# Kernel tuning notes

Measured on AMD Instinct MI355X. Metric: run time of the kernel, lower is better.

## Reference

```python
import jax, jax.numpy as jnp
import numpy as np

QLEN, B, D = 1024, 4, 512
H, DH = 8, 64
MEM, DMLP = 1024, 2048
KLEN = MEM + QLEN
EPS = 1e-5


def layer_norm(x, g, b):
    mu = jnp.mean(x, axis=-1, keepdims=True)
    var = jnp.var(x, axis=-1, keepdims=True)
    return (x - mu) * jax.lax.rsqrt(var + EPS) * g + b


def rel_shift(x):
    # x: [qlen, klen, b, h] -- Transformer-XL relative shift trick
    q, k, b, h = x.shape
    zp = jnp.zeros((q, 1, b, h), dtype=x.dtype)
    x = jnp.concatenate([zp, x], axis=1)          # [q, k+1, b, h]
    x = x.reshape(k + 1, q, b, h)[1:]             # drop first row
    return x.reshape(q, k, b, h)


def setup_inputs() -> dict:
    key = jax.random.key(0)
    ks = jax.random.split(key, 12)
    s = 0.02
    inp = {
        "inputs": jax.random.normal(ks[0], (QLEN, B, D), jnp.float32),
        "r": jax.random.normal(ks[1], (KLEN, D), jnp.float32),
        "u": jax.random.normal(ks[2], (H, DH), jnp.float32) * s,
        "v": jax.random.normal(ks[3], (H, DH), jnp.float32) * s,
        "mem": jax.random.normal(ks[4], (MEM, B, D), jnp.float32),
        # causal mask: query i (global pos MEM+i) cannot attend key j > MEM+i
        "attn_mask": jnp.arange(KLEN)[None, :] > (jnp.arange(QLEN)[:, None] + MEM),
        "Wqkv": jax.random.normal(ks[5], (3 * D, D), jnp.float32) * s,
        "Wr": jax.random.normal(ks[6], (D, D), jnp.float32) * s,
        "Wo": jax.random.normal(ks[7], (D, D), jnp.float32) * s,
        "ln1_g": jnp.ones((D,), jnp.float32),
        "ln1_b": jnp.zeros((D,), jnp.float32),
        "mlp_w1": jax.random.normal(ks[8], (DMLP, D), jnp.float32) * s,
        "mlp_b1": jnp.zeros((DMLP,), jnp.float32),
        "mlp_w2": jax.random.normal(ks[9], (D, DMLP), jnp.float32) * s,
        "mlp_b2": jnp.zeros((D,), jnp.float32),
        "ln2_g": jnp.ones((D,), jnp.float32),
        "ln2_b": jnp.zeros((D,), jnp.float32),
    }
    return inp


def reference(inputs, r, u, v, mem, attn_mask, Wqkv, Wr, Wo,
              ln1_g, ln1_b, mlp_w1, mlp_b1, mlp_w2, mlp_b2, ln2_g, ln2_b):
    qlen, b, d = inputs.shape
    cat = jnp.concatenate([mem, inputs], axis=0)          # [klen, b, d]
    klen = cat.shape[0]
    qkv = cat @ Wqkv.T                                    # [klen, b, 3d]
    q, k, w_v = jnp.split(qkv, 3, axis=-1)
    q = q[-qlen:].reshape(qlen, b, H, DH)
    k = k.reshape(klen, b, H, DH)
    w_v = w_v.reshape(klen, b, H, DH)
    rk = (r @ Wr.T).reshape(klen, H, DH)                  # [klen, h, dh]

    AC = jnp.einsum('ibhd,jbhd->ijbh', q + u, k)          # content term
    BD = jnp.einsum('ibhd,jhd->ijbh', q + v, rk)          # position term
    BD = rel_shift(BD)
    scale = 1.0 / np.sqrt(DH)
    score = (AC + BD) * scale                             # [q, k, b, h]
    score = jnp.where(attn_mask[:, :, None, None], jnp.float32(-1e30), score)
    prob = jax.nn.softmax(score, axis=1)
    attn = jnp.einsum('ijbh,jbhd->ibhd', prob, w_v).reshape(qlen, b, d)
    attn_out = attn @ Wo.T

    y = layer_norm(inputs + attn_out, ln1_g, ln1_b)
    h = jax.nn.relu(y @ mlp_w1.T + mlp_b1)
    z = h @ mlp_w2.T + mlp_b2
    out = layer_norm(y + z, ln2_g, ln2_b)
    return out, prob
```

## Files before the change

kernel.cpp:

```cpp
#include <hip/hip_runtime.h>
#include <math.h>

#define QL 1024
#define BSZ 4
#define DM 512
#define NH 8
#define DHH 64
#define MEML 1024
#define KL 2048
#define DMLP 2048

typedef __attribute__((ext_vector_type(8))) short bf16x8;
typedef __attribute__((ext_vector_type(4))) float f32x4;

#define MFMA16(A, B, C) __builtin_amdgcn_mfma_f32_16x16x32_bf16((A), (B), (C), 0, 0, 0)
#define SWZB(r, cb) (((r) << 7) + ((cb) ^ (((r) & 7) << 4)))
#define RINGB(r, c) (((r) << 9) + ((((c) << 2)) ^ (((r) & 7) << 4)))
#define CVT2(dst, lo, hi) \
  asm("v_cvt_pk_bf16_f32 %0, %1, %2" : "=v"(dst) : "v"(lo), "v"(hi))
#define GLOAD_LDS(gp, lp) __builtin_amdgcn_global_load_lds( \
    (const __attribute__((address_space(1))) void*)(gp), \
    (__attribute__((address_space(3))) void*)(lp), 16, 0, 0)

__device__ __forceinline__ unsigned short bf16_1(float x) {
  unsigned int t; CVT2(t, x, x); return (unsigned short)t;
}
__device__ __forceinline__ void split1(float x, unsigned short& h, unsigned short& l) {
  unsigned int th; CVT2(th, x, x);
  h = (unsigned short)th;
  const float r = x - __uint_as_float(((unsigned int)h) << 16);
  unsigned int tl; CVT2(tl, r, r);
  l = (unsigned short)tl;
}

__device__ __forceinline__ void split_bf16(const float4 a, uint2& h, uint2& l) {
  CVT2(h.x, a.x, a.y); CVT2(h.y, a.z, a.w);
  float r;
  float4 rr;
  rr.x = a.x - __uint_as_float(h.x << 16);
  rr.y = a.y - __uint_as_float(h.x & 0xffff0000u);
  rr.z = a.z - __uint_as_float(h.y << 16);
  rr.w = a.w - __uint_as_float(h.y & 0xffff0000u);
  CVT2(l.x, rr.x, rr.y); CVT2(l.y, rr.z, rr.w);
  (void)r;
}

__device__ __forceinline__ void store_tiled(char* hiB, char* loB, int KT,
                                            int row, int c0, uint2 h, uint2 l) {
  const size_t off = (((size_t)(row >> 7) * KT + (c0 >> 6)) << 14)
                   + SWZB(row & 127, (c0 & 63) * 2);
  *(uint2*)(hiB + off) = h;
  *(uint2*)(loB + off) = l;
}

__global__ __launch_bounds__(256)
void precvt_all(const float* __restrict__ mem, const float* __restrict__ inputs,
                const float* __restrict__ r, const float* __restrict__ Wqkv,
                const float* __restrict__ Wr, const float* __restrict__ Wo,
                const float* __restrict__ w1, const float* __restrict__ w2,
                unsigned short* CAThi, unsigned short* CATlo,
                unsigned short* Rhi, unsigned short* Rlo,
                unsigned short* Qhi, unsigned short* Qlo,
                unsigned short* WrHi, unsigned short* WrLo,
                unsigned short* WoHi, unsigned short* WoLo,
                unsigned short* w1Hi, unsigned short* w1Lo,
                unsigned short* w2Hi, unsigned short* w2Lo) {
  const int id = blockIdx.x * 256 + threadIdx.x;
  float4 a; uint2 h, l;
  if (id < 1048576) {
    const int row = id >> 7, c0 = (id & 127) * 4;
    const float* s = (row < 4096) ? mem + (size_t)row * 512
                                  : inputs + (size_t)(row - 4096) * 512;
    a = *(const float4*)(s + c0);
    split_bf16(a, h, l);
    store_tiled((char*)CAThi, (char*)CATlo, 8, row, c0, h, l);
  } else if (id < 1310720) {
    const int e = id - 1048576, row = e >> 7, c0 = (e & 127) * 4;
    a = *(const float4*)(r + (size_t)row * 512 + c0);
    split_bf16(a, h, l);
    store_tiled((char*)Rhi, (char*)Rlo, 8, row, c0, h, l);
  } else if (id < 1507328) {
    const int e = id - 1310720, row = e >> 7, c0 = (e & 127) * 4;
    a = *(const float4*)(Wqkv + (size_t)row * 512 + c0);
    split_bf16(a, h, l);
    store_tiled((char*)Qhi, (char*)Qlo, 8, row, c0, h, l);
  } else if (id < 1572864) {
    const int e = id - 1507328, row = e >> 7, c0 = (e & 127) * 4;
    a = *(const float4*)(Wr + (size_t)row * 512 + c0);
    split_bf16(a, h, l);
    store_tiled((char*)WrHi, (char*)WrLo, 8, row, c0, h, l);
  } else if (id < 1638400) {
    const int e = id - 1572864, row = e >> 7, c0 = (e & 127) * 4;
    a = *(const float4*)(Wo + (size_t)row * 512 + c0);
    split_bf16(a, h, l);
    store_tiled((char*)WoHi, (char*)WoLo, 8, row, c0, h, l);
  } else if (id < 1900544) {
    const int e = id - 1638400, row = e >> 7, c0 = (e & 127) * 4;
    a = *(const float4*)(w1 + (size_t)row * 512 + c0);
    split_bf16(a, h, l);
    store_tiled((char*)w1Hi, (char*)w1Lo, 8, row, c0, h, l);
  } else if (id < 2162688) {
    const int e = id - 1900544, row = e >> 9, c0 = (e & 511) * 4;
    a = *(const float4*)(w2 + (size_t)row * 2048 + c0);
    split_bf16(a, h, l);
    store_tiled((char*)w2Hi, (char*)w2Lo, 32, row, c0, h, l);
  }
}

template<int BM, int EPI, bool BIAS, bool RELU>
__global__ __launch_bounds__(256)
void gemm_nt_mfma(const unsigned short* __restrict__ AhiT, const unsigned short* __restrict__ AloT,
                  const unsigned short* __restrict__ WhiT, const unsigned short* __restrict__ WloT,
                  const float* __restrict__ bias,
                  float* __restrict__ C,
                  unsigned short* __restrict__ X1, unsigned short* __restrict__ X2,
                  int N, int K, int KTC) {
  constexpr int MR = 4;
  constexpr int NR = (BM == 128) ? 4 : 2;
  __shared__ __align__(16) unsigned short Ahi[BM * 64];
  __shared__ __align__(16) unsigned short Alo[BM * 64];
  __shared__ __align__(16) unsigned short Bhi[128 * 64];
  __shared__ __align__(16) unsigned short Blo[128 * 64];

  const int t = threadIdx.x;
  const int w = t >> 6, lane = t & 63;
  const int lq = lane & 15, lg = lane >> 4;
  const int row0 = blockIdx.y * BM, col0 = blockIdx.x * 128;
  const int wrow0 = (BM == 128) ? (w >> 1) * 64 : 0;
  const int wcol0 = (BM == 128) ? (w & 1) * 64 : w * 32;
  const int KT = K >> 6;
  const size_t amt = (size_t)(row0 >> 7) * KT;
  const int asub = (row0 & 127) << 7;
  const size_t bnt = (size_t)(col0 >> 7) * KT;

  f32x4 acc[MR][NR];
  #pragma unroll
  for (int m = 0; m < MR; ++m)
    #pragma unroll
    for (int n = 0; n < NR; ++n)
      acc[m][n] = (f32x4){0.f, 0.f, 0.f, 0.f};

  for (int kt = 0; kt < KT; ++kt) {
    __syncthreads();
    {
      const char* gbh = (const char*)WhiT + ((bnt + kt) << 14);
      const char* gbl = (const char*)WloT + ((bnt + kt) << 14);
      #pragma unroll
      for (int i = 0; i < 4; ++i) {
        const int off = (w * 4 + i) * 1024;
        GLOAD_LDS(gbh + off + lane * 16, (char*)Bhi + off);
        GLOAD_LDS(gbl + off + lane * 16, (char*)Blo + off);
      }
    }
    {
      const char* gah = (const char*)AhiT + ((amt + kt) << 14) + asub;
      const char* gal = (const char*)AloT + ((amt + kt) << 14) + asub;
      #pragma unroll
      for (int i = 0; i < BM / 32; ++i) {
        const int off = (w * (BM / 32) + i) * 1024;
        GLOAD_LDS(gah + off + lane * 16, (char*)Ahi + off);
        GLOAD_LDS(gal + off + lane * 16, (char*)Alo + off);
      }
    }
    __syncthreads();
    #pragma unroll
    for (int ks = 0; ks < 2; ++ks) {
      bf16x8 ah[MR], al[MR], bh[NR], bl[NR];
      #pragma unroll
      for (int m = 0; m < MR; ++m) {
        ah[m] = *(const bf16x8*)((const char*)Ahi + SWZB(wrow0 + m * 16 + lq, ks * 64 + lg * 16));
        al[m] = *(const bf16x8*)((const char*)Alo + SWZB(wrow0 + m * 16 + lq, ks * 64 + lg * 16));
      }
      #pragma unroll
      for (int n = 0; n < NR; ++n) {
        bh[n] = *(const bf16x8*)((const char*)Bhi + SWZB(wcol0 + n * 16 + lq, ks * 64 + lg * 16));
        bl[n] = *(const bf16x8*)((const char*)Blo + SWZB(wcol0 + n * 16 + lq, ks * 64 + lg * 16));
      }
      #pragma unroll
      for (int m = 0; m < MR; ++m)
        #pragma unroll
        for (int n = 0; n < NR; ++n) {
          acc[m][n] = MFMA16(ah[m], bh[n], acc[m][n]);
          acc[m][n] = MFMA16(ah[m], bl[n], acc[m][n]);
          acc[m][n] = MFMA16(al[m], bh[n], acc[m][n]);
        }
    }
  }
  #pragma unroll
  for (int n = 0; n < NR; ++n) {
    const int col = col0 + wcol0 + n * 16 + lq;
    const float bv = BIAS ? bias[col] : 0.f;
    #pragma unroll
    for (int m = 0; m < MR; ++m) {
      #pragma unroll
      for (int rg = 0; rg < 4; ++rg) {
        const int row = row0 + wrow0 + m * 16 + lg * 4 + rg;
        float vv = acc[m][n][rg] + bv;
        if (RELU) vv = fmaxf(vv, 0.f);
        if constexpr (EPI == 0) {
          C[(size_t)row * N + col] = vv;
        } else if constexpr (EPI == 1) {
          const int j = row >> 2, b = row & 3;
          if (col0 < 512) {
            C[(size_t)row * 512 + col] = vv;
          } else if (col0 < 1024) {
            const int hh = (col - 512) >> 6, d = (col - 512) & 63;
            const size_t off = (((size_t)((b * 8 + hh) * 32 + (j >> 6))) << 13)
                             + SWZB(j & 63, d * 2);
            *(unsigned short*)((char*)X1 + off) = bf16_1(vv);
          } else {
            const int hh = (col - 1024) >> 6, d = (col - 1024) & 63;
            const size_t off = (((size_t)((b * 8 + hh) * 32 + (j >> 6))) << 13)
                             + d * 128 + (j & 63) * 2;
            *(unsigned short*)((char*)X2 + off) = bf16_1(vv);
          }
        } else if constexpr (EPI == 2) {
          const int hh = col >> 6, d = col & 63;
          const size_t off = (((size_t)(hh * 32 + (row >> 6))) << 13)
                           + SWZB(row & 63, d * 2);
          *(unsigned short*)((char*)X1 + off) = bf16_1(vv);
        } else {
          unsigned short hh, ll;
          split1(vv, hh, ll);
          const size_t off = (((size_t)(row >> 7) * KTC + (col >> 6)) << 14)
                           + SWZB(row & 127, (col & 63) * 2);
          *(unsigned short*)((char*)X1 + off) = hh;
          *(unsigned short*)((char*)X2 + off) = ll;
        }
      }
    }
  }
}

__global__ __launch_bounds__(256)
void attn3_kernel(const float* __restrict__ Qbuf,
                  const unsigned short* __restrict__ Kb,
                  const unsigned short* __restrict__ Rb,
                  const unsigned short* __restrict__ Vtb,
                  const float* __restrict__ u, const float* __restrict__ v,
                  unsigned short* __restrict__ P, float* __restrict__ INV,
                  unsigned short* __restrict__ AThiT, unsigned short* __restrict__ ATloT) {
  const int b = blockIdx.y;
  const int h = blockIdx.z;
  const int i0 = (((h >> 2) & 1) ? (15 - (int)blockIdx.x) : (int)blockIdx.x) * 64;
  const int t = threadIdx.x;
  const int w = t >> 6;
  const int lane = t & 63;
  const int lq = lane & 15;
  const int lg = lane >> 4;
  const int bh = b * 8 + h;

  __shared__ __align__(16) unsigned short Ks[2][4096];
  __shared__ __align__(16) unsigned short Rs[2][4096];
  __shared__ __align__(16) unsigned short Es[4096];
  __shared__ __align__(16) float Ring[8192];

  const int ntiles = i0 / 64 + 17;

  auto dma = [&](int jt, int jrt, int buf) {
    const char* gk = (const char*)Kb + (((size_t)bh * 32 + jt) << 13);
    const char* gr = (const char*)Rb + (((size_t)h * 32 + jrt) << 13);
    const int off = w * 2048;
    GLOAD_LDS(gk + off + lane * 16, (char*)Ks[buf] + off);
    GLOAD_LDS(gk + off + 1024 + lane * 16, (char*)Ks[buf] + off + 1024);
    GLOAD_LDS(gr + off + lane * 16, (char*)Rs[buf] + off);
    GLOAD_LDS(gr + off + 1024 + lane * 16, (char*)Rs[buf] + off + 1024);
  };

  dma(0, (1024 - i0) >> 6, 0);
  {
    const int jrtp = (960 - i0) >> 6;
    const char* gr = (const char*)Rb + (((size_t)h * 32 + jrtp) << 13);
    const int off = w * 2048;
    GLOAD_LDS(gr + off + lane * 16, (char*)Rs[1] + off);
    GLOAD_LDS(gr + off + 1024 + lane * 16, (char*)Rs[1] + off + 1024);
  }
  #pragma unroll
  for (int it = 0; it < 4; ++it) {
    const int idx = it * 256 + t;
    const int row = idx >> 4, c4 = (idx & 15) * 4;
    const float4 q4 = *(const float4*)(Qbuf + ((size_t)(MEML + i0 + row) * 4 + b) * 512 + h * 64 + c4);
    const float4 u4 = *(const float4*)(u + h * 64 + c4);
    const float4 v4 = *(const float4*)(v + h * 64 + c4);
    uint2 qp;
    CVT2(qp.x, q4.x + u4.x, q4.y + u4.y); CVT2(qp.y, q4.z + u4.z, q4.w + u4.w);
    *(uint2*)((char*)Es + SWZB(row, c4 * 2)) = qp;
    CVT2(qp.x, q4.x + v4.x, q4.y + v4.y); CVT2(qp.y, q4.z + v4.z, q4.w + v4.w);
    *(uint2*)((char*)Ks[1] + SWZB(row, c4 * 2)) = qp;
  }
  __syncthreads();

  const bf16x8 qu0 = *(const bf16x8*)((const char*)Es + SWZB(w * 16 + lq, lg * 16));
  const bf16x8 qu1 = *(const bf16x8*)((const char*)Es + SWZB(w * 16 + lq, 64 + lg * 16));
  const bf16x8 qv0 = *(const bf16x8*)((const char*)Ks[1] + SWZB(w * 16 + lq, lg * 16));
  const bf16x8 qv1 = *(const bf16x8*)((const char*)Ks[1] + SWZB(w * 16 + lq, 64 + lg * 16));

  {
    f32x4 bd[4];
    #pragma unroll
    for (int nj = 0; nj < 4; ++nj) bd[nj] = (f32x4){0.f, 0.f, 0.f, 0.f};
    #pragma unroll
    for (int nj = 0; nj < 4; ++nj) {
      const bf16x8 rf0 = *(const bf16x8*)((const char*)Rs[1] + SWZB(nj * 16 + lq, lg * 16));
      const bf16x8 rf1 = *(const bf16x8*)((const char*)Rs[1] + SWZB(nj * 16 + lq, 64 + lg * 16));
      bd[nj] = MFMA16(qv0, rf0, bd[nj]);
      bd[nj] = MFMA16(qv1, rf1, bd[nj]);
    }
    #pragma unroll
    for (int nj = 0; nj < 4; ++nj) {
      const int jrl = nj * 16 + lq;
      #pragma unroll
      for (int rg = 0; rg < 4; ++rg) {
        const int il = w * 16 + lg * 4 + rg;
        *(float*)((char*)Ring + RINGB(il, 64 + jrl)) = bd[nj][rg];
      }
    }
  }

  f32x4 pv[4];
  #pragma unroll
  for (int nd = 0; nd < 4; ++nd) pv[nd] = (f32x4){0.f, 0.f, 0.f, 0.f};
  float rs[4] = {0.f, 0.f, 0.f, 0.f};

  for (int n = 0; n < ntiles; ++n) {
    const int j0 = n * 64;
    const int cur = n & 1;
    __syncthreads();
    const char* gv = (const char*)Vtb + (((size_t)bh * 32 + n) << 13);
    bf16x8 vf0[4], vf1[4];
    #pragma unroll
    for (int nd = 0; nd < 4; ++nd) {
      vf0[nd] = *(const bf16x8*)(gv + (nd * 16 + lq) * 128 + lg * 16);
      vf1[nd] = *(const bf16x8*)(gv + (nd * 16 + lq) * 128 + 64 + lg * 16);
    }
    if (n + 1 < ntiles) {
      int jrt = ((n + 1) * 64 - i0 + 1024) >> 6;
      if (jrt > 31) jrt = 31;
      dma(n + 1, jrt, cur ^ 1);
    }
    const char* KsB = (const char*)Ks[cur];
    const char* RsB = (const char*)Rs[cur];
    f32x4 acc[4], bdn[4];
    #pragma unroll
    for (int nj = 0; nj < 4; ++nj) {
      acc[nj] = (f32x4){0.f, 0.f, 0.f, 0.f};
      bdn[nj] = (f32x4){0.f, 0.f, 0.f, 0.f};
    }
    #pragma unroll
    for (int nj = 0; nj < 4; ++nj) {
      const bf16x8 kf0 = *(const bf16x8*)(KsB + SWZB(nj * 16 + lq, lg * 16));
      const bf16x8 rf0 = *(const bf16x8*)(RsB + SWZB(nj * 16 + lq, lg * 16));
      acc[nj] = MFMA16(qu0, kf0, acc[nj]);
      bdn[nj] = MFMA16(qv0, rf0, bdn[nj]);
      const bf16x8 kf1 = *(const bf16x8*)(KsB + SWZB(nj * 16 + lq, 64 + lg * 16));
      const bf16x8 rf1 = *(const bf16x8*)(RsB + SWZB(nj * 16 + lq, 64 + lg * 16));
      acc[nj] = MFMA16(qu1, kf1, acc[nj]);
      bdn[nj] = MFMA16(qv1, rf1, bdn[nj]);
    }
    const int base_cur = cur * 64;
    const int base_prev = 64 - base_cur;
    #pragma unroll
    for (int nj = 0; nj < 4; ++nj) {
      const int jrl = nj * 16 + lq;
      #pragma unroll
      for (int rg = 0; rg < 4; ++rg) {
        const int il = w * 16 + lg * 4 + rg;
        *(float*)((char*)Ring + RINGB(il, base_cur + jrl)) = bdn[nj][rg];
      }
    }
    const bool lastm = (n == ntiles - 1);
    #pragma unroll
    for (int njp = 0; njp < 2; ++njp) {
      #pragma unroll
      for (int rg = 0; rg < 4; ++rg) {
        const int il = w * 16 + lg * 4 + rg;
        float ee[2];
        #pragma unroll
        for (int q2 = 0; q2 < 2; ++q2) {
          const int nj = njp * 2 + q2;
          const int jl = nj * 16 + lq;
          const int jr_rel = jl - il + 63;
          const float ringv = (jr_rel < 64)
              ? *(const float*)((const char*)Ring + RINGB(il, base_prev + jr_rel))
              : *(const float*)((const char*)Ring + RINGB(il, base_cur + jr_rel - 64));
          const float s = 0.125f * (acc[nj][rg] + ringv);
          float e = __expf(s);
          if (lastm && jl > il) e = 0.f;
          rs[rg] += e;
          ee[q2] = e;
        }
        unsigned int pk2; CVT2(pk2, ee[0], ee[1]);
        const int jlA = (njp * 2) * 16 + lq;
        *(unsigned short*)((char*)Es + SWZB(il, jlA * 2)) = (unsigned short)(pk2 & 0xffffu);
        *(unsigned short*)((char*)Es + SWZB(il, (jlA + 16) * 2)) = (unsigned short)(pk2 >> 16);
      }
    }
    {
      const bf16x8 pf0 = *(const bf16x8*)((const char*)Es + SWZB(w * 16 + lq, lg * 16));
      const bf16x8 pf1 = *(const bf16x8*)((const char*)Es + SWZB(w * 16 + lq, 64 + lg * 16));
      #pragma unroll
      for (int nd = 0; nd < 4; ++nd) {
        pv[nd] = MFMA16(pf0, vf0[nd], pv[nd]);
        pv[nd] = MFMA16(pf1, vf1[nd], pv[nd]);
      }
    }
    #pragma unroll
    for (int it = 0; it < 2; ++it) {
      const int lin = it * 64 + lane;
      const int rr = lin >> 3, c16 = lin & 7;
      const int row = w * 16 + rr;
      const uint4 val = *(const uint4*)((const char*)Es + SWZB(row, c16 * 16));
      *(uint4*)(P + ((size_t)bh * 1024 + i0 + row) * 2048 + j0 + c16 * 8) = val;
    }
  }

  #pragma unroll
  for (int rg = 0; rg < 4; ++rg) {
    #pragma unroll
    for (int m = 1; m < 16; m <<= 1) rs[rg] += __shfl_xor(rs[rg], m, 64);
  }
  float inv[4];
  #pragma unroll
  for (int rg = 0; rg < 4; ++rg) inv[rg] = 1.0f / rs[rg];
  if (lq == 0) {
    #pragma unroll
    for (int rg = 0; rg < 4; ++rg)
      INV[(size_t)bh * 1024 + i0 + w * 16 + lg * 4 + rg] = inv[rg];
  }
  #pragma unroll
  for (int nd = 0; nd < 4; ++nd) {
    const int col = h * 64 + nd * 16 + lq;
    #pragma unroll
    for (int rg = 0; rg < 4; ++rg) {
      const int row = (i0 + w * 16 + lg * 4 + rg) * 4 + b;
      unsigned short hh, ll;
      split1(pv[nd][rg] * inv[rg], hh, ll);
      const size_t off = (((size_t)(row >> 7) * 8 + (col >> 6)) << 14)
                       + SWZB(row & 127, (col & 63) * 2);
      *(unsigned short*)((char*)AThiT + off) = hh;
      *(unsigned short*)((char*)ATloT + off) = ll;
    }
  }
}

__global__ __launch_bounds__(256)
void ptrans_kernel(const unsigned short* __restrict__ P, const float* __restrict__ INV,
                   float* __restrict__ prob) {
  const int i  = blockIdx.x;
  const int j0 = blockIdx.y * 64;
  const int t  = threadIdx.x;
  __shared__ float tile[32][65];
  __shared__ float invs[32];
  const bool valid = j0 <= (i & ~63) + MEML;
  if (t < 32) invs[t] = INV[(size_t)t * 1024 + i];
  if (valid) {
    const int bh = t >> 3, part = t & 7;
    const uint4 raw = *(const uint4*)(P + ((size_t)bh * 1024 + i) * 2048 + j0 + part * 8);
    const unsigned int w[4] = {raw.x, raw.y, raw.z, raw.w};
    #pragma unroll
    for (int k = 0; k < 4; ++k) {
      tile[bh][part*8 + 2*k]     = __uint_as_float(w[k] << 16);
      tile[bh][part*8 + 2*k + 1] = __uint_as_float(w[k] & 0xffff0000u);
    }
  }
  __syncthreads();
  #pragma unroll
  for (int it = 0; it < 8; ++it) {
    const int idx = it * 256 + t;
    const int jl = idx >> 5, bh = idx & 31;
    const float val = valid ? tile[bh][jl] * invs[bh] : 0.f;
    prob[((size_t)i * 2048 + j0 + jl) * 32 + bh] = val;
  }
}

template<bool SPLIT>
__global__ __launch_bounds__(256)
void ln_res_kernel(const float* __restrict__ xa, const float* __restrict__ xb,
                   const float* __restrict__ g, const float* __restrict__ bb,
                   float* __restrict__ y,
                   unsigned short* __restrict__ YhiT, unsigned short* __restrict__ YloT) {
  const int rrow = blockIdx.x;
  const int t = threadIdx.x;
  const size_t base = (size_t)rrow * DM;
  __shared__ float red[256];
  const float a0 = xa[base + t]       + xb[base + t];
  const float a1 = xa[base + t + 256] + xb[base + t + 256];
  red[t] = a0 + a1; __syncthreads();
  for (int s = 128; s > 0; s >>= 1) { if (t < s) red[t] += red[t+s]; __syncthreads(); }
  const float mu = red[0] * (1.0f/512.0f);
  __syncthreads();
  red[t] = a0*a0 + a1*a1; __syncthreads();
  for (int s = 128; s > 0; s >>= 1) { if (t < s) red[t] += red[t+s]; __syncthreads(); }
  const float var = red[0] * (1.0f/512.0f) - mu*mu;
  const float w = rsqrtf(var + 1e-5f);
  const float y0 = (a0 - mu) * w * g[t]       + bb[t];
  const float y1 = (a1 - mu) * w * g[t + 256] + bb[t + 256];
  y[base + t]       = y0;
  y[base + t + 256] = y1;
  if (SPLIT) {
    unsigned short hh, ll;
    split1(y0, hh, ll);
    size_t off = (((size_t)(rrow >> 7) * 8 + (t >> 6)) << 14)
               + SWZB(rrow & 127, (t & 63) * 2);
    *(unsigned short*)((char*)YhiT + off) = hh;
    *(unsigned short*)((char*)YloT + off) = ll;
    split1(y1, hh, ll);
    const int t2 = t + 256;
    off = (((size_t)(rrow >> 7) * 8 + (t2 >> 6)) << 14)
        + SWZB(rrow & 127, (t2 & 63) * 2);
    *(unsigned short*)((char*)YhiT + off) = hh;
    *(unsigned short*)((char*)YloT + off) = ll;
  }
}

extern "C" void kernel_launch(void* const* d_in, const int* in_sizes, int n_in,
                              void* d_out, int out_size, void* d_ws, size_t ws_size,
                              hipStream_t stream) {
  const float* inputs = (const float*)d_in[0];
  const float* r      = (const float*)d_in[1];
  const float* u      = (const float*)d_in[2];
  const float* v      = (const float*)d_in[3];
  const float* mem    = (const float*)d_in[4];
  const float* Wqkv   = (const float*)d_in[6];
  const float* Wr     = (const float*)d_in[7];
  const float* Wo     = (const float*)d_in[8];
  const float* ln1g   = (const float*)d_in[9];
  const float* ln1b   = (const float*)d_in[10];
  const float* w1     = (const float*)d_in[11];
  const float* b1     = (const float*)d_in[12];
  const float* w2     = (const float*)d_in[13];
  const float* b2     = (const float*)d_in[14];
  const float* ln2g   = (const float*)d_in[15];
  const float* ln2b   = (const float*)d_in[16];

  float* out  = (float*)d_out;
  float* prob = out + (size_t)QL*BSZ*DM;

  float* ws   = (float*)d_ws;
  unsigned short* P = (unsigned short*)ws;

  unsigned short* CAThiT = (unsigned short*)ws;
  unsigned short* CATloT = CAThiT + 4194304;
  unsigned short* RinhiT = CATloT + 4194304;
  unsigned short* RinloT = RinhiT + 1048576;
  unsigned short* WqhiT  = RinloT + 1048576;
  unsigned short* WqloT  = WqhiT + 786432;
  unsigned short* WrhiT  = WqloT + 786432;
  unsigned short* WrloT  = WrhiT + 262144;
  unsigned short* HMhiT = (unsigned short*)ws;
  unsigned short* HMloT = HMhiT + 8388608;
  float* Z = ws + 8388608;

  float* Qbuf = ws + 33554432;
  float* AO   = Qbuf + 4194304;
  float* Y    = AO + 2097152;
  float* INV  = Y + 2097152;
  unsigned short* AThiT = (unsigned short*)(INV + 32768);
  unsigned short* ATloT = AThiT + 2097152;
  unsigned short* YhiT  = ATloT + 2097152;
  unsigned short* YloT  = YhiT + 2097152;
  unsigned short* WohiT = YloT + 2097152;
  unsigned short* WoloT = WohiT + 262144;
  unsigned short* w1hiT = WoloT + 262144;
  unsigned short* w1loT = w1hiT + 1048576;
  unsigned short* w2hiT = w1loT + 1048576;
  unsigned short* w2loT = w2hiT + 1048576;
  unsigned short* Kb    = w2loT + 1048576;
  unsigned short* Vtb   = Kb + 4194304;
  unsigned short* Rb    = Vtb + 4194304;

  const dim3 blk256(256);

  precvt_all<<<dim3(8448), blk256, 0, stream>>>(
      mem, inputs, r, Wqkv, Wr, Wo, w1, w2,
      CAThiT, CATloT, RinhiT, RinloT, WqhiT, WqloT, WrhiT, WrloT,
      WohiT, WoloT, w1hiT, w1loT, w2hiT, w2loT);

  gemm_nt_mfma<128,1,false,false><<<dim3(12, 64), blk256, 0, stream>>>(
      CAThiT, CATloT, WqhiT, WqloT, nullptr, Qbuf, Kb, Vtb, 1536, 512, 0);
  gemm_nt_mfma<64,2,false,false><<<dim3(4, 32), blk256, 0, stream>>>(
      RinhiT, RinloT, WrhiT, WrloT, nullptr, nullptr, Rb, nullptr, 512, 512, 0);
  attn3_kernel<<<dim3(16, BSZ, NH), blk256, 0, stream>>>(
      Qbuf, Kb, Rb, Vtb, u, v, P, INV, AThiT, ATloT);
  ptrans_kernel<<<dim3(1024, 32), blk256, 0, stream>>>(P, INV, prob);

  gemm_nt_mfma<64,0,false,false><<<dim3(4, 64), blk256, 0, stream>>>(
      AThiT, ATloT, WohiT, WoloT, nullptr, AO, nullptr, nullptr, 512, 512, 0);
  ln_res_kernel<true><<<dim3(4096), blk256, 0, stream>>>(
      inputs, AO, ln1g, ln1b, Y, YhiT, YloT);
  gemm_nt_mfma<128,3,true,true><<<dim3(16, 32), blk256, 0, stream>>>(
      YhiT, YloT, w1hiT, w1loT, b1, nullptr, HMhiT, HMloT, 2048, 512, 32);
  gemm_nt_mfma<64,0,true,false><<<dim3(4, 64), blk256, 0, stream>>>(
      HMhiT, HMloT, w2hiT, w2loT, b2, Z, nullptr, nullptr, 512, 2048, 0);
  ln_res_kernel<false><<<dim3(4096), blk256, 0, stream>>>(
      Y, Z, ln2g, ln2b, out, nullptr, nullptr);
}
```

Baseline: 656.4 us.

## Load K/R fragments directly from global memory instead of LDS double-buffering

The attention kernel no longer stages K and R tiles into shared memory with async global-to-LDS copies and double buffering. Each wave now reads its MFMA fragments straight from global (L2-cached) memory, and the upstream GEMM epilogues write K and R in an unswizzled row layout to match. Q+u/Q+v fragments are built in registers directly, removing the prologue LDS staging and its barrier. The per-tile __syncthreads is dropped and s_setprio is raised around the MFMA blocks. This cuts LDS use and barriers, but may expose global-load latency with no prefetch, and shared Es/Ring reuse without barriers could race.

```diff
diff --git a/kernel.cpp b/kernel.cpp
--- a/kernel.cpp
+++ b/kernel.cpp
@@ -35,14 +35,12 @@
 
 __device__ __forceinline__ void split_bf16(const float4 a, uint2& h, uint2& l) {
   CVT2(h.x, a.x, a.y); CVT2(h.y, a.z, a.w);
-  float r;
   float4 rr;
   rr.x = a.x - __uint_as_float(h.x << 16);
   rr.y = a.y - __uint_as_float(h.x & 0xffff0000u);
   rr.z = a.z - __uint_as_float(h.y << 16);
   rr.w = a.w - __uint_as_float(h.y & 0xffff0000u);
   CVT2(l.x, rr.x, rr.y); CVT2(l.y, rr.z, rr.w);
-  (void)r;
 }
 
 __device__ __forceinline__ void store_tiled(char* hiB, char* loB, int KT,
@@ -206,7 +204,7 @@
           } else if (col0 < 1024) {
             const int hh = (col - 512) >> 6, d = (col - 512) & 63;
             const size_t off = (((size_t)((b * 8 + hh) * 32 + (j >> 6))) << 13)
-                             + SWZB(j & 63, d * 2);
+                             + (j & 63) * 128 + d * 2;
             *(unsigned short*)((char*)X1 + off) = bf16_1(vv);
           } else {
             const int hh = (col - 1024) >> 6, d = (col - 1024) & 63;
@@ -217,7 +215,7 @@
         } else if constexpr (EPI == 2) {
           const int hh = col >> 6, d = col & 63;
           const size_t off = (((size_t)(hh * 32 + (row >> 6))) << 13)
-                           + SWZB(row & 63, d * 2);
+                           + (row & 63) * 128 + d * 2;
           *(unsigned short*)((char*)X1 + off) = bf16_1(vv);
         } else {
           unsigned short hh, ll;
@@ -233,7 +231,7 @@
 }
 
 __global__ __launch_bounds__(256)
-void attn3_kernel(const float* __restrict__ Qbuf,
+void attn4_kernel(const float* __restrict__ Qbuf,
                   const unsigned short* __restrict__ Kb,
                   const unsigned short* __restrict__ Rb,
                   const unsigned short* __restrict__ Vtb,
@@ -250,59 +248,44 @@
   const int lg = lane >> 4;
   const int bh = b * 8 + h;
 
-  __shared__ __align__(16) unsigned short Ks[2][4096];
-  __shared__ __align__(16) unsigned short Rs[2][4096];
   __shared__ __align__(16) unsigned short Es[4096];
   __shared__ __align__(16) float Ring[8192];
 
   const int ntiles = i0 / 64 + 17;
 
-  auto dma = [&](int jt, int jrt, int buf) {
-    const char* gk = (const char*)Kb + (((size_t)bh * 32 + jt) << 13);
-    const char* gr = (const char*)Rb + (((size_t)h * 32 + jrt) << 13);
-    const int off = w * 2048;
-    GLOAD_LDS(gk + off + lane * 16, (char*)Ks[buf] + off);
-    GLOAD_LDS(gk + off + 1024 + lane * 16, (char*)Ks[buf] + off + 1024);
-    GLOAD_LDS(gr + off + lane * 16, (char*)Rs[buf] + off);
-    GLOAD_LDS(gr + off + 1024 + lane * 16, (char*)Rs[buf] + off + 1024);
-  };
-
-  dma(0, (1024 - i0) >> 6, 0);
+  bf16x8 qu0, qu1, qv0, qv1;
   {
-    const int jrtp = (960 - i0) >> 6;
-    const char* gr = (const char*)Rb + (((size_t)h * 32 + jrtp) << 13);
-    const int off = w * 2048;
-    GLOAD_LDS(gr + off + lane * 16, (char*)Rs[1] + off);
-    GLOAD_LDS(gr + off + 1024 + lane * 16, (char*)Rs[1] + off + 1024);
-  }
-  #pragma unroll
-  for (int it = 0; it < 4; ++it) {
-    const int idx = it * 256 + t;
-    const int row = idx >> 4, c4 = (idx & 15) * 4;
-    const float4 q4 = *(const float4*)(Qbuf + ((size_t)(MEML + i0 + row) * 4 + b) * 512 + h * 64 + c4);
-    const float4 u4 = *(const float4*)(u + h * 64 + c4);
-    const float4 v4 = *(const float4*)(v + h * 64 + c4);
-    uint2 qp;
-    CVT2(qp.x, q4.x + u4.x, q4.y + u4.y); CVT2(qp.y, q4.z + u4.z, q4.w + u4.w);
-    *(uint2*)((char*)Es + SWZB(row, c4 * 2)) = qp;
-    CVT2(qp.x, q4.x + v4.x, q4.y + v4.y); CVT2(qp.y, q4.z + v4.z, q4.w + v4.w);
-    *(uint2*)((char*)Ks[1] + SWZB(row, c4 * 2)) = qp;
-  }
-  __syncthreads();
-
-  const bf16x8 qu0 = *(const bf16x8*)((const char*)Es + SWZB(w * 16 + lq, lg * 16));
-  const bf16x8 qu1 = *(const bf16x8*)((const char*)Es + SWZB(w * 16 + lq, 64 + lg * 16));
-  const bf16x8 qv0 = *(const bf16x8*)((const char*)Ks[1] + SWZB(w * 16 + lq, lg * 16));
-  const bf16x8 qv1 = *(const bf16x8*)((const char*)Ks[1] + SWZB(w * 16 + lq, 64 + lg * 16));
+    const float* qrow = Qbuf + ((size_t)(MEML + i0 + w * 16 + lq) * 4 + b) * 512 + h * 64;
+    const float* up = u + h * 64;
+    const float* vp = v + h * 64;
+    #pragma unroll
+    for (int half = 0; half < 2; ++half) {
+      const int d0 = half * 32 + lg * 8;
+      const float4 a0 = *(const float4*)(qrow + d0);
+      const float4 a1 = *(const float4*)(qrow + d0 + 4);
+      const float4 ua = *(const float4*)(up + d0);
+      const float4 ub = *(const float4*)(up + d0 + 4);
+      const float4 va = *(const float4*)(vp + d0);
+      const float4 vb = *(const float4*)(vp + d0 + 4);
+      uint4 uu, vv;
+      CVT2(uu.x, a0.x + ua.x, a0.y + ua.y); CVT2(uu.y, a0.z + ua.z, a0.w + ua.w);
+      CVT2(uu.z, a1.x + ub.x, a1.y + ub.y); CVT2(uu.w, a1.z + ub.z, a1.w + ub.w);
+      CVT2(vv.x, a0.x + va.x, a0.y + va.y); CVT2(vv.y, a0.z + va.z, a0.w + va.w);
+      CVT2(vv.z, a1.x + vb.x, a1.y + vb.y); CVT2(vv.w, a1.z + vb.z, a1.w + vb.w);
+      if (half == 0) { qu0 = *(bf16x8*)&uu; qv0 = *(bf16x8*)&vv; }
+      else           { qu1 = *(bf16x8*)&uu; qv1 = *(bf16x8*)&vv; }
+    }
+  }
 
   {
+    const char* gr = (const char*)Rb + (((size_t)(h * 32 + ((960 - i0) >> 6))) << 13);
     f32x4 bd[4];
     #pragma unroll
     for (int nj = 0; nj < 4; ++nj) bd[nj] = (f32x4){0.f, 0.f, 0.f, 0.f};
     #pragma unroll
     for (int nj = 0; nj < 4; ++nj) {
-      const bf16x8 rf0 = *(const bf16x8*)((const char*)Rs[1] + SWZB(nj * 16 + lq, lg * 16));
-      const bf16x8 rf1 = *(const bf16x8*)((const char*)Rs[1] + SWZB(nj * 16 + lq, 64 + lg * 16));
+      const bf16x8 rf0 = *(const bf16x8*)(gr + (nj * 16 + lq) * 128 + lg * 16);
+      const bf16x8 rf1 = *(const bf16x8*)(gr + (nj * 16 + lq) * 128 + 64 + lg * 16);
       bd[nj] = MFMA16(qv0, rf0, bd[nj]);
       bd[nj] = MFMA16(qv1, rf1, bd[nj]);
     }
@@ -324,40 +307,39 @@
 
   for (int n = 0; n < ntiles; ++n) {
     const int j0 = n * 64;
-    const int cur = n & 1;
-    __syncthreads();
-    const char* gv = (const char*)Vtb + (((size_t)bh * 32 + n) << 13);
+    const char* gk = (const char*)Kb + (((size_t)(bh * 32 + n)) << 13);
+    int jrt = (j0 - i0 + 1024) >> 6;
+    if (jrt > 31) jrt = 31;
+    const char* gr = (const char*)Rb + (((size_t)(h * 32 + jrt)) << 13);
+    const char* gv = (const char*)Vtb + (((size_t)(bh * 32 + n)) << 13);
+
     bf16x8 vf0[4], vf1[4];
     #pragma unroll
     for (int nd = 0; nd < 4; ++nd) {
       vf0[nd] = *(const bf16x8*)(gv + (nd * 16 + lq) * 128 + lg * 16);
       vf1[nd] = *(const bf16x8*)(gv + (nd * 16 + lq) * 128 + 64 + lg * 16);
     }
-    if (n + 1 < ntiles) {
-      int jrt = ((n + 1) * 64 - i0 + 1024) >> 6;
-      if (jrt > 31) jrt = 31;
-      dma(n + 1, jrt, cur ^ 1);
-    }
-    const char* KsB = (const char*)Ks[cur];
-    const char* RsB = (const char*)Rs[cur];
     f32x4 acc[4], bdn[4];
     #pragma unroll
     for (int nj = 0; nj < 4; ++nj) {
       acc[nj] = (f32x4){0.f, 0.f, 0.f, 0.f};
       bdn[nj] = (f32x4){0.f, 0.f, 0.f, 0.f};
     }
+    __builtin_amdgcn_s_setprio(1);
     #pragma unroll
     for (int nj = 0; nj < 4; ++nj) {
-      const bf16x8 kf0 = *(const bf16x8*)(KsB + SWZB(nj * 16 + lq, lg * 16));
-      const bf16x8 rf0 = *(const bf16x8*)(RsB + SWZB(nj * 16 + lq, lg * 16));
+      const int rowb = (nj * 16 + lq) * 128;
+      const bf16x8 kf0 = *(const bf16x8*)(gk + rowb + lg * 16);
+      const bf16x8 rf0 = *(const bf16x8*)(gr + rowb + lg * 16);
       acc[nj] = MFMA16(qu0, kf0, acc[nj]);
       bdn[nj] = MFMA16(qv0, rf0, bdn[nj]);
-      const bf16x8 kf1 = *(const bf16x8*)(KsB + SWZB(nj * 16 + lq, 64 + lg * 16));
-      const bf16x8 rf1 = *(const bf16x8*)(RsB + SWZB(nj * 16 + lq, 64 + lg * 16));
+      const bf16x8 kf1 = *(const bf16x8*)(gk + rowb + 64 + lg * 16);
+      const bf16x8 rf1 = *(const bf16x8*)(gr + rowb + 64 + lg * 16);
       acc[nj] = MFMA16(qu1, kf1, acc[nj]);
       bdn[nj] = MFMA16(qv1, rf1, bdn[nj]);
     }
-    const int base_cur = cur * 64;
+    __builtin_amdgcn_s_setprio(0);
+    const int base_cur = (n & 1) * 64;
     const int base_prev = 64 - base_cur;
     #pragma unroll
     for (int nj = 0; nj < 4; ++nj) {
@@ -398,11 +380,13 @@
     {
       const bf16x8 pf0 = *(const bf16x8*)((const char*)Es + SWZB(w * 16 + lq, lg * 16));
       const bf16x8 pf1 = *(const bf16x8*)((const char*)Es + SWZB(w * 16 + lq, 64 + lg * 16));
+      __builtin_amdgcn_s_setprio(1);
       #pragma unroll
       for (int nd = 0; nd < 4; ++nd) {
         pv[nd] = MFMA16(pf0, vf0[nd], pv[nd]);
         pv[nd] = MFMA16(pf1, vf1[nd], pv[nd]);
       }
+      __builtin_amdgcn_s_setprio(0);
     }
     #pragma unroll
     for (int it = 0; it < 2; ++it) {
@@ -580,7 +564,7 @@
       CAThiT, CATloT, WqhiT, WqloT, nullptr, Qbuf, Kb, Vtb, 1536, 512, 0);
   gemm_nt_mfma<64,2,false,false><<<dim3(4, 32), blk256, 0, stream>>>(
       RinhiT, RinloT, WrhiT, WrloT, nullptr, nullptr, Rb, nullptr, 512, 512, 0);
-  attn3_kernel<<<dim3(16, BSZ, NH), blk256, 0, stream>>>(
+  attn4_kernel<<<dim3(16, BSZ, NH), blk256, 0, stream>>>(
       Qbuf, Kb, Rb, Vtb, u, v, P, INV, AThiT, ATloT);
   ptrans_kernel<<<dim3(1024, 32), blk256, 0, stream>>>(P, INV, prob);
 
```

Result: slower. 716.7 us (+9.2%).
